# Optimization experiments

Measured on AMD Instinct MI355X. Metric: run time of the kernel, lower is better.

## Reference

```python
import jax, jax.numpy as jnp
import numpy as np

D_MODEL = 1024
N_HEADS = 16
HEAD_DIM = D_MODEL // N_HEADS


def setup_inputs() -> dict:
    key = jax.random.key(0)
    ks = jax.random.split(key, 5)
    scale = 1.0 / np.sqrt(D_MODEL)
    return {
        "x": jax.random.normal(ks[0], (4, 2048, D_MODEL), dtype=jnp.float32),
        "W_q": jax.random.normal(ks[1], (D_MODEL, D_MODEL), dtype=jnp.float32) * scale,
        "W_k": jax.random.normal(ks[2], (D_MODEL, D_MODEL), dtype=jnp.float32) * scale,
        "W_v": jax.random.normal(ks[3], (D_MODEL, D_MODEL), dtype=jnp.float32) * scale,
        "W_o": jax.random.normal(ks[4], (D_MODEL, D_MODEL), dtype=jnp.float32) * scale,
    }


def _split_heads(t):
    # (B, T, d_model) -> (B, H, T, head_dim)
    B, T, _ = t.shape
    return t.reshape(B, T, N_HEADS, HEAD_DIM).transpose(0, 2, 1, 3)


def reference(x, W_q, W_k, W_v, W_o):
    B, T, _ = x.shape
    # torch nn.Linear: y = x @ W.T
    q = _split_heads(x @ W_q.T)
    k = _split_heads(x @ W_k.T)
    v = _split_heads(x @ W_v.T)
    scale = jnp.asarray(np.sqrt(HEAD_DIM), x.dtype)
    # (B, H, T, T) scores, additive causal mask (triu above diagonal = -inf)
    scores = jnp.einsum("bhqd,bhkd->bhqk", q, k) / scale
    causal = jnp.tril(jnp.ones((T, T), dtype=bool))
    scores = jnp.where(causal, scores, jnp.asarray(-jnp.inf, scores.dtype))
    weights = jax.nn.softmax(scores, axis=-1)
    out = jnp.einsum("bhqk,bhkd->bhqd", weights, v)
    out = out.transpose(0, 2, 1, 3).reshape(B, T, D_MODEL)
    out = out @ W_o.T
    return out, k, v
```

## Files before the change

### kernel.cpp

```cpp
#include <hip/hip_runtime.h>
#include <stdint.h>

typedef __bf16 bf16;
typedef __bf16 bf16x8 __attribute__((ext_vector_type(8)));
typedef __bf16 bf16x4 __attribute__((ext_vector_type(4)));
typedef short short4v __attribute__((ext_vector_type(4)));
typedef float f32x4 __attribute__((ext_vector_type(4)));
typedef int v2i __attribute__((ext_vector_type(2)));
typedef uint32_t u32;

#define MFMA_BF16(a, b, c) __builtin_amdgcn_mfma_f32_16x16x32_bf16(a, b, c, 0, 0, 0)
#define MFMA16(a, b, c)                                                   \
  __builtin_amdgcn_mfma_f32_16x16x16bf16_1k(*(const short4v*)&(a),        \
                                            *(const short4v*)&(b), c, 0, 0, 0)

#define TRREAD(dst, va, IMM)                                             \
  asm volatile("ds_read_b64_tr_b16 %0, %1 offset:" #IMM                  \
               : "=v"(dst)                                               \
               : "v"(va))

constexpr int D_MODEL = 1024;
constexpr int T_SEQ = 2048;
constexpr int NH = 16;
constexpr int HD = 64;
constexpr size_t OUT_ELEMS = (size_t)4 * T_SEQ * D_MODEL;
constexpr size_t X_ELEMS = OUT_ELEMS;
constexpr size_t W_ELEMS = (size_t)D_MODEL * D_MODEL;

__device__ __forceinline__ void gload16(const bf16* g, bf16* l) {
  __builtin_amdgcn_global_load_lds(
      (const __attribute__((address_space(1))) unsigned int*)g,
      (__attribute__((address_space(3))) unsigned int*)l, 16, 0, 0);
}

__global__ __launch_bounds__(256) void convert_kernel(
    const float* __restrict__ x, const float* __restrict__ wq,
    const float* __restrict__ wk, const float* __restrict__ wv,
    const float* __restrict__ wo, bf16* __restrict__ dst,
    bf16* __restrict__ wo_b) {
  const size_t nchunk = (X_ELEMS + 4 * W_ELEMS) / 8;
  for (size_t c = (size_t)blockIdx.x * 256 + threadIdx.x; c < nchunk;
       c += (size_t)gridDim.x * 256) {
    const size_t off = c * 8;
    const float* src;
    bf16* d;
    size_t rel;
    if (off < X_ELEMS) {
      src = x;
      rel = off;
      d = dst + off;
    } else {
      const size_t j = off - X_ELEMS;
      const int w = (int)(j >> 20);
      rel = j & (W_ELEMS - 1);
      if (w == 3) {
        if (!wo_b) continue;
        src = wo;
        d = wo_b + rel;
      } else {
        src = (w == 0) ? wq : (w == 1) ? wk : wv;
        d = dst + off;
      }
    }
    const f32x4 a = *(const f32x4*)(src + rel);
    const f32x4 b = *(const f32x4*)(src + rel + 4);
    bf16x8 o;
#pragma unroll
    for (int e = 0; e < 4; ++e) {
      o[e] = (bf16)a[e];
      o[e + 4] = (bf16)b[e];
    }
    *(bf16x8*)d = o;
  }
}

template <bool B_F32>
__global__ __launch_bounds__(256) void gemm2(
    const bf16* __restrict__ A, const bf16* __restrict__ WB,
    const float* __restrict__ WF, int modeBase, bf16* __restrict__ dstB,
    float* __restrict__ dstF1, float* __restrict__ dstF2) {
  const int z = blockIdx.z;
  const int mode = modeBase + z;
  const bf16* Bb = B_F32 ? nullptr : WB + (size_t)z * W_ELEMS;
  const int m0 = blockIdx.y * 128, n0 = blockIdx.x * 128;
  const int tid = threadIdx.x;
  const int wave = tid >> 6, lane = tid & 63;
  const int quad = lane >> 4, c16 = lane & 15;
  const int wr = wave >> 1, wc = wave & 1;

  __shared__ __align__(16) bf16 As[128 * 64];
  __shared__ __align__(16) bf16 Bs[128 * 64];

  f32x4 acc[4][4];
#pragma unroll
  for (int i = 0; i < 4; ++i)
#pragma unroll
    for (int j = 0; j < 4; ++j) acc[i][j] = (f32x4){0.f, 0.f, 0.f, 0.f};

  const int r8 = lane >> 3;
  const int s8 = lane & 7;
  const int ksw = ((s8 ^ r8) * 8);
  const int swA = (c16 & 7);

  for (int k0 = 0; k0 < 1024; k0 += 64) {
    __syncthreads();
#pragma unroll
    for (int c = 0; c < 4; ++c) {
      const int chunk = wave + c * 4;
      const int row = chunk * 8 + r8;
      gload16(A + (size_t)(m0 + row) * 1024 + k0 + ksw, &As[chunk * 512]);
      if (!B_F32)
        gload16(Bb + (size_t)(n0 + row) * 1024 + k0 + ksw, &Bs[chunk * 512]);
    }
    if (B_F32) {
#pragma unroll
      for (int g = 0; g < 4; ++g) {
        const int gi = g * 256 + tid;
        const int row = gi >> 3, s = gi & 7;
        const float* bp = WF + (size_t)(n0 + row) * 1024 + k0 + s * 8;
        const f32x4 b0 = *(const f32x4*)bp;
        const f32x4 b1 = *(const f32x4*)(bp + 4);
        bf16x8 vb;
#pragma unroll
        for (int e = 0; e < 4; ++e) {
          vb[e] = (bf16)b0[e];
          vb[e + 4] = (bf16)b1[e];
        }
        *(bf16x8*)&Bs[row * 64 + ((s ^ (row & 7)) * 8)] = vb;
      }
    }
    asm volatile("s_waitcnt vmcnt(0)" ::: "memory");
    __syncthreads();

#pragma unroll
    for (int kk = 0; kk < 2; ++kk) {
      bf16x8 af[4], bfr[4];
#pragma unroll
      for (int i = 0; i < 4; ++i) {
        const int row = wr * 64 + i * 16 + c16;
        af[i] = *(const bf16x8*)&As[row * 64 + (((quad + kk * 4) ^ swA) * 8)];
      }
#pragma unroll
      for (int j = 0; j < 4; ++j) {
        const int row = wc * 64 + j * 16 + c16;
        bfr[j] = *(const bf16x8*)&Bs[row * 64 + (((quad + kk * 4) ^ swA) * 8)];
      }
#pragma unroll
      for (int i = 0; i < 4; ++i)
#pragma unroll
        for (int j = 0; j < 4; ++j)
          acc[i][j] = MFMA_BF16(af[i], bfr[j], acc[i][j]);
    }
  }

  const int row0 = m0 + wr * 64, col0 = n0 + wc * 64;
#pragma unroll
  for (int i = 0; i < 4; ++i) {
#pragma unroll
    for (int r = 0; r < 4; ++r) {
      const int row = row0 + i * 16 + quad * 4 + r;
      const int b = row >> 11, t = row & 2047;
#pragma unroll
      for (int j = 0; j < 4; ++j) {
        const int cc = col0 + j * 16 + c16;
        const float v = acc[i][j][r];
        if (mode == 0) {
          dstB[(size_t)row * 1024 + cc] = (bf16)v;
        } else if (mode == 3) {
          dstF1[(size_t)row * 1024 + cc] = v;
        } else {
          const int h = cc >> 6, d = cc & 63;
          float* df = (mode == 1) ? dstF1 : dstF2;
          df[((size_t)(b * NH + h) * T_SEQ + t) * HD + d] = v;
        }
      }
    }
  }
}

__device__ __forceinline__ void load_kv(const float* Kg, const float* Vg,
                                        int t0, int st, int sd,
                                        f32x4 pk[2][2], f32x4 pv[2][2]) {
#pragma unroll
  for (int p = 0; p < 2; ++p) {
    const float* kp = Kg + (size_t)(t0 + p * 32 + st) * HD + sd * 8;
    pk[p][0] = *(const f32x4*)kp;
    pk[p][1] = *(const f32x4*)(kp + 4);
    const float* vp = Vg + (size_t)(t0 + p * 32 + st) * HD + sd * 8;
    pv[p][0] = *(const f32x4*)vp;
    pv[p][1] = *(const f32x4*)(vp + 4);
  }
}

__global__ __launch_bounds__(256, 4) void attn_kernel(
    const bf16* __restrict__ Q, const float* __restrict__ K,
    const float* __restrict__ V, bf16* __restrict__ Aout) {
  const int bx = blockIdx.x;
  const int by = blockIdx.y;
  const int r16 = (bx + ((by >> 4) << 2)) & 15;
  const int qt = (r16 < 8) ? r16 : 23 - r16;
  const int b = by >> 4, h = by & 15;
  const int tid = threadIdx.x, wave = tid >> 6, lane = tid & 63;
  const int quad = lane >> 4, c16 = lane & 15;

  __shared__ __align__(16) bf16 Ks[64 * 70];
  __shared__ __align__(16) bf16 Vs[4096];

  const int q0w = qt * 128 + wave * 32;
  const bf16* Qb = Q + ((size_t)b * T_SEQ + q0w) * D_MODEL + h * HD;
  const float* Kg = K + (size_t)by * T_SEQ * HD;
  const float* Vg = V + (size_t)by * T_SEQ * HD;

  bf16x8 aq[2][2];
#pragma unroll
  for (int mt = 0; mt < 2; ++mt) {
    const bf16* qp = Qb + (size_t)(mt * 16 + c16) * D_MODEL + quad * 8;
    aq[mt][0] = *(const bf16x8*)qp;
    aq[mt][1] = *(const bf16x8*)(qp + 32);
  }

  f32x4 O[2][4], racc[2];
#pragma unroll
  for (int mt = 0; mt < 2; ++mt) {
    racc[mt] = (f32x4){0.f, 0.f, 0.f, 0.f};
#pragma unroll
    for (int dj = 0; dj < 4; ++dj) O[mt][dj] = (f32x4){0.f, 0.f, 0.f, 0.f};
  }

  bf16x4 ones4;
#pragma unroll
  for (int e = 0; e < 4; ++e) ones4[e] = (bf16)1.0f;

  const float sc = 0.125f * 1.44269504088896340736f;
  const int nkt = 2 * qt + 2;
  const int st = tid >> 3, sd = tid & 7;
  const u32 vtr =
      (u32)(uintptr_t)(const __attribute__((address_space(3))) bf16*)Vs +
      (u32)lane * 8;

  f32x4 pk[2][2], pv[2][2];
  load_kv(Kg, Vg, 0, st, sd, pk, pv);

  for (int kt = 0; kt < nkt; ++kt) {
    const int t0 = kt * 64;

    __syncthreads();
#pragma unroll
    for (int p = 0; p < 2; ++p) {
      const int t = p * 32 + st;
      bf16x8 kb, vb;
#pragma unroll
      for (int e = 0; e < 4; ++e) {
        kb[e] = (bf16)pk[p][0][e];
        kb[e + 4] = (bf16)pk[p][1][e];
        vb[e] = (bf16)pv[p][0][e];
        vb[e + 4] = (bf16)pv[p][1][e];
      }
      *(bf16x8*)&Ks[t * 70 + sd * 8] = kb;
      *(bf16x8*)&Vs[(((t >> 4) * 4 + (sd >> 1)) * 256) + (t & 15) * 16 +
                    (sd & 1) * 8] = vb;
    }
    if (kt + 1 < nkt) load_kv(Kg, Vg, t0 + 64, st, sd, pk, pv);
    __syncthreads();

    const bool act[2] = {t0 <= q0w + 15, t0 <= q0w + 31};

    bf16x4 ap16[2][4];
#pragma unroll
    for (int j = 0; j < 4; ++j) {
      const bf16* kp = &Ks[(j * 16 + c16) * 70 + quad * 8];
      const bf16x8 ak0 = *(const bf16x8*)kp;
      const bf16x8 ak1 = *(const bf16x8*)(kp + 32);
#pragma unroll
      for (int mt = 0; mt < 2; ++mt) {
        if (!act[mt]) continue;
        f32x4 s = (f32x4){0.f, 0.f, 0.f, 0.f};
        s = MFMA_BF16(ak0, aq[mt][0], s);
        s = MFMA_BF16(ak1, aq[mt][1], s);
        const int trow = t0 + j * 16 + quad * 4;
        const int qcol = q0w + mt * 16 + c16;
        bf16x4 pa;
#pragma unroll
        for (int r = 0; r < 4; ++r)
          pa[r] = (bf16)((trow + r <= qcol) ? exp2f(s[r] * sc) : 0.f);
        ap16[mt][j] = pa;
      }
    }

    if (act[1]) {
#pragma unroll
      for (int mt = 0; mt < 2; ++mt) {
        if (!act[mt]) continue;
#pragma unroll
        for (int j = 0; j < 4; ++j)
          racc[mt] = MFMA16(ap16[mt][j], ones4, racc[mt]);
      }
      v2i bv0, bv1, bv2, bv3;
#define PV_DJ(DJ, O0, O1, O2, O3)                                        \
  {                                                                      \
    TRREAD(bv0, vtr, O0);                                                \
    TRREAD(bv1, vtr, O1);                                                \
    TRREAD(bv2, vtr, O2);                                                \
    TRREAD(bv3, vtr, O3);                                                \
    asm volatile("s_waitcnt lgkmcnt(0)" ::: "memory");                   \
    __builtin_amdgcn_sched_barrier(0);                                   \
    _Pragma("unroll") for (int mt = 0; mt < 2; ++mt) {                   \
      if (act[mt]) {                                                     \
        O[mt][DJ] = MFMA16(ap16[mt][0], bv0, O[mt][DJ]);                 \
        O[mt][DJ] = MFMA16(ap16[mt][1], bv1, O[mt][DJ]);                 \
        O[mt][DJ] = MFMA16(ap16[mt][2], bv2, O[mt][DJ]);                 \
        O[mt][DJ] = MFMA16(ap16[mt][3], bv3, O[mt][DJ]);                 \
      }                                                                  \
    }                                                                    \
  }
      PV_DJ(0, 0, 2048, 4096, 6144)
      PV_DJ(1, 512, 2560, 4608, 6656)
      PV_DJ(2, 1024, 3072, 5120, 7168)
      PV_DJ(3, 1536, 3584, 5632, 7680)
#undef PV_DJ
    }
  }

#pragma unroll
  for (int mt = 0; mt < 2; ++mt) {
    f32x4 inv;
#pragma unroll
    for (int r = 0; r < 4; ++r) inv[r] = 1.f / racc[mt][r];
#pragma unroll
    for (int dj = 0; dj < 4; ++dj)
#pragma unroll
      for (int r = 0; r < 4; ++r) {
        const int q = q0w + mt * 16 + quad * 4 + r;
        Aout[((size_t)b * T_SEQ + q) * D_MODEL + h * HD + dj * 16 + c16] =
            (bf16)(O[mt][dj][r] * inv[r]);
      }
  }
}

extern "C" void kernel_launch(void* const* d_in, const int* in_sizes, int n_in,
                              void* d_out, int out_size, void* d_ws, size_t ws_size,
                              hipStream_t stream) {
  const float* x = (const float*)d_in[0];
  const float* wq = (const float*)d_in[1];
  const float* wk = (const float*)d_in[2];
  const float* wv = (const float*)d_in[3];
  const float* wo = (const float*)d_in[4];

  float* out = (float*)d_out;
  float* kout = out + OUT_ELEMS;
  float* vout = out + 2 * OUT_ELEMS;

  bf16* ws = (bf16*)d_ws;
  bf16* Qbuf = ws;
  bf16* Abuf = ws;

  bf16* cvt = (bf16*)d_out;
  const bf16* xb = cvt;
  const bf16* wb = cvt + X_ELEMS;

  const bool wo_bf = ws_size >= (X_ELEMS + W_ELEMS) * sizeof(bf16);
  bf16* wo_b = wo_bf ? (ws + X_ELEMS) : nullptr;

  convert_kernel<<<dim3(2048), 256, 0, stream>>>(x, wq, wk, wv, wo, cvt, wo_b);
  gemm2<false><<<dim3(8, 64, 3), 256, 0, stream>>>(xb, wb, nullptr, 0, Qbuf,
                                                   kout, vout);
  attn_kernel<<<dim3(16, 64), 256, 0, stream>>>(Qbuf, kout, vout, Abuf);
  if (wo_bf) {
    gemm2<false><<<dim3(8, 64, 1), 256, 0, stream>>>(Abuf, wo_b, nullptr, 3,
                                                     nullptr, out, nullptr);
  } else {
    gemm2<true><<<dim3(8, 64, 1), 256, 0, stream>>>(Abuf, nullptr, wo, 3,
                                                    nullptr, out, nullptr);
  }
}
```

Before: 377.0 us.

## Split attention block into 8 waves of 16 query rows with MFMA priority

Raises the attention block from 256 to 512 threads so each wave owns 16 query rows instead of 32, and each thread stages a single K/V row chunk per tile. This halves per-wave register state (O, ap16, prefetch buffers) and adds more waves to hide latency, including finer-grained causal skipping per 16-row wave. It also raises wave priority around the MFMA section with s_setprio. The cost is that each K/V tile in LDS is reused by fewer rows per wave, more waves wait at each barrier, and the explicit occupancy hint is dropped.

```diff
diff --git a/kernel.cpp b/kernel.cpp
--- a/kernel.cpp
+++ b/kernel.cpp
@@ -178,21 +178,7 @@
   }
 }
 
-__device__ __forceinline__ void load_kv(const float* Kg, const float* Vg,
-                                        int t0, int st, int sd,
-                                        f32x4 pk[2][2], f32x4 pv[2][2]) {
-#pragma unroll
-  for (int p = 0; p < 2; ++p) {
-    const float* kp = Kg + (size_t)(t0 + p * 32 + st) * HD + sd * 8;
-    pk[p][0] = *(const f32x4*)kp;
-    pk[p][1] = *(const f32x4*)(kp + 4);
-    const float* vp = Vg + (size_t)(t0 + p * 32 + st) * HD + sd * 8;
-    pv[p][0] = *(const f32x4*)vp;
-    pv[p][1] = *(const f32x4*)(vp + 4);
-  }
-}
-
-__global__ __launch_bounds__(256, 4) void attn_kernel(
+__global__ __launch_bounds__(512) void attn_kernel(
     const bf16* __restrict__ Q, const float* __restrict__ K,
     const float* __restrict__ V, bf16* __restrict__ Aout) {
   const int bx = blockIdx.x;
@@ -206,26 +192,21 @@
   __shared__ __align__(16) bf16 Ks[64 * 70];
   __shared__ __align__(16) bf16 Vs[4096];
 
-  const int q0w = qt * 128 + wave * 32;
-  const bf16* Qb = Q + ((size_t)b * T_SEQ + q0w) * D_MODEL + h * HD;
+  const int q0w = qt * 128 + wave * 16;
   const float* Kg = K + (size_t)by * T_SEQ * HD;
   const float* Vg = V + (size_t)by * T_SEQ * HD;
 
-  bf16x8 aq[2][2];
-#pragma unroll
-  for (int mt = 0; mt < 2; ++mt) {
-    const bf16* qp = Qb + (size_t)(mt * 16 + c16) * D_MODEL + quad * 8;
-    aq[mt][0] = *(const bf16x8*)qp;
-    aq[mt][1] = *(const bf16x8*)(qp + 32);
-  }
-
-  f32x4 O[2][4], racc[2];
-#pragma unroll
-  for (int mt = 0; mt < 2; ++mt) {
-    racc[mt] = (f32x4){0.f, 0.f, 0.f, 0.f};
-#pragma unroll
-    for (int dj = 0; dj < 4; ++dj) O[mt][dj] = (f32x4){0.f, 0.f, 0.f, 0.f};
-  }
+  bf16x8 aq[2];
+  {
+    const bf16* qp =
+        Q + ((size_t)b * T_SEQ + q0w + c16) * D_MODEL + h * HD + quad * 8;
+    aq[0] = *(const bf16x8*)qp;
+    aq[1] = *(const bf16x8*)(qp + 32);
+  }
+
+  f32x4 O[4], racc = (f32x4){0.f, 0.f, 0.f, 0.f};
+#pragma unroll
+  for (int dj = 0; dj < 4; ++dj) O[dj] = (f32x4){0.f, 0.f, 0.f, 0.f};
 
   bf16x4 ones4;
 #pragma unroll
@@ -238,63 +219,65 @@
       (u32)(uintptr_t)(const __attribute__((address_space(3))) bf16*)Vs +
       (u32)lane * 8;
 
-  f32x4 pk[2][2], pv[2][2];
-  load_kv(Kg, Vg, 0, st, sd, pk, pv);
+  f32x4 pk[2], pv[2];
+  {
+    const float* kp = Kg + (size_t)st * HD + sd * 8;
+    pk[0] = *(const f32x4*)kp;
+    pk[1] = *(const f32x4*)(kp + 4);
+    const float* vp = Vg + (size_t)st * HD + sd * 8;
+    pv[0] = *(const f32x4*)vp;
+    pv[1] = *(const f32x4*)(vp + 4);
+  }
 
   for (int kt = 0; kt < nkt; ++kt) {
     const int t0 = kt * 64;
 
     __syncthreads();
-#pragma unroll
-    for (int p = 0; p < 2; ++p) {
-      const int t = p * 32 + st;
+    {
       bf16x8 kb, vb;
 #pragma unroll
       for (int e = 0; e < 4; ++e) {
-        kb[e] = (bf16)pk[p][0][e];
-        kb[e + 4] = (bf16)pk[p][1][e];
-        vb[e] = (bf16)pv[p][0][e];
-        vb[e + 4] = (bf16)pv[p][1][e];
-      }
-      *(bf16x8*)&Ks[t * 70 + sd * 8] = kb;
-      *(bf16x8*)&Vs[(((t >> 4) * 4 + (sd >> 1)) * 256) + (t & 15) * 16 +
+        kb[e] = (bf16)pk[0][e];
+        kb[e + 4] = (bf16)pk[1][e];
+        vb[e] = (bf16)pv[0][e];
+        vb[e + 4] = (bf16)pv[1][e];
+      }
+      *(bf16x8*)&Ks[st * 70 + sd * 8] = kb;
+      *(bf16x8*)&Vs[(((st >> 4) * 4 + (sd >> 1)) * 256) + (st & 15) * 16 +
                     (sd & 1) * 8] = vb;
     }
-    if (kt + 1 < nkt) load_kv(Kg, Vg, t0 + 64, st, sd, pk, pv);
+    if (kt + 1 < nkt) {
+      const float* kp = Kg + (size_t)(t0 + 64 + st) * HD + sd * 8;
+      pk[0] = *(const f32x4*)kp;
+      pk[1] = *(const f32x4*)(kp + 4);
+      const float* vp = Vg + (size_t)(t0 + 64 + st) * HD + sd * 8;
+      pv[0] = *(const f32x4*)vp;
+      pv[1] = *(const f32x4*)(vp + 4);
+    }
     __syncthreads();
 
-    const bool act[2] = {t0 <= q0w + 15, t0 <= q0w + 31};
-
-    bf16x4 ap16[2][4];
-#pragma unroll
-    for (int j = 0; j < 4; ++j) {
-      const bf16* kp = &Ks[(j * 16 + c16) * 70 + quad * 8];
-      const bf16x8 ak0 = *(const bf16x8*)kp;
-      const bf16x8 ak1 = *(const bf16x8*)(kp + 32);
-#pragma unroll
-      for (int mt = 0; mt < 2; ++mt) {
-        if (!act[mt]) continue;
+    if (t0 <= q0w + 15) {
+      bf16x4 ap16[4];
+#pragma unroll
+      for (int j = 0; j < 4; ++j) {
+        const bf16* kp = &Ks[(j * 16 + c16) * 70 + quad * 8];
+        const bf16x8 ak0 = *(const bf16x8*)kp;
+        const bf16x8 ak1 = *(const bf16x8*)(kp + 32);
         f32x4 s = (f32x4){0.f, 0.f, 0.f, 0.f};
-        s = MFMA_BF16(ak0, aq[mt][0], s);
-        s = MFMA_BF16(ak1, aq[mt][1], s);
+        s = MFMA_BF16(ak0, aq[0], s);
+        s = MFMA_BF16(ak1, aq[1], s);
         const int trow = t0 + j * 16 + quad * 4;
-        const int qcol = q0w + mt * 16 + c16;
+        const int qcol = q0w + c16;
         bf16x4 pa;
 #pragma unroll
         for (int r = 0; r < 4; ++r)
           pa[r] = (bf16)((trow + r <= qcol) ? exp2f(s[r] * sc) : 0.f);
-        ap16[mt][j] = pa;
-      }
-    }
-
-    if (act[1]) {
-#pragma unroll
-      for (int mt = 0; mt < 2; ++mt) {
-        if (!act[mt]) continue;
-#pragma unroll
-        for (int j = 0; j < 4; ++j)
-          racc[mt] = MFMA16(ap16[mt][j], ones4, racc[mt]);
-      }
+        ap16[j] = pa;
+      }
+
+      __builtin_amdgcn_s_setprio(1);
+#pragma unroll
+      for (int j = 0; j < 4; ++j) racc = MFMA16(ap16[j], ones4, racc);
       v2i bv0, bv1, bv2, bv3;
 #define PV_DJ(DJ, O0, O1, O2, O3)                                        \
   {                                                                      \
@@ -304,37 +287,31 @@
     TRREAD(bv3, vtr, O3);                                                \
     asm volatile("s_waitcnt lgkmcnt(0)" ::: "memory");                   \
     __builtin_amdgcn_sched_barrier(0);                                   \
-    _Pragma("unroll") for (int mt = 0; mt < 2; ++mt) {                   \
-      if (act[mt]) {                                                     \
-        O[mt][DJ] = MFMA16(ap16[mt][0], bv0, O[mt][DJ]);                 \
-        O[mt][DJ] = MFMA16(ap16[mt][1], bv1, O[mt][DJ]);                 \
-        O[mt][DJ] = MFMA16(ap16[mt][2], bv2, O[mt][DJ]);                 \
-        O[mt][DJ] = MFMA16(ap16[mt][3], bv3, O[mt][DJ]);                 \
-      }                                                                  \
-    }                                                                    \
+    O[DJ] = MFMA16(ap16[0], bv0, O[DJ]);                                 \
+    O[DJ] = MFMA16(ap16[1], bv1, O[DJ]);                                 \
+    O[DJ] = MFMA16(ap16[2], bv2, O[DJ]);                                 \
+    O[DJ] = MFMA16(ap16[3], bv3, O[DJ]);                                 \
   }
       PV_DJ(0, 0, 2048, 4096, 6144)
       PV_DJ(1, 512, 2560, 4608, 6656)
       PV_DJ(2, 1024, 3072, 5120, 7168)
       PV_DJ(3, 1536, 3584, 5632, 7680)
 #undef PV_DJ
-    }
-  }
-
-#pragma unroll
-  for (int mt = 0; mt < 2; ++mt) {
-    f32x4 inv;
-#pragma unroll
-    for (int r = 0; r < 4; ++r) inv[r] = 1.f / racc[mt][r];
-#pragma unroll
-    for (int dj = 0; dj < 4; ++dj)
-#pragma unroll
-      for (int r = 0; r < 4; ++r) {
-        const int q = q0w + mt * 16 + quad * 4 + r;
-        Aout[((size_t)b * T_SEQ + q) * D_MODEL + h * HD + dj * 16 + c16] =
-            (bf16)(O[mt][dj][r] * inv[r]);
-      }
-  }
+      __builtin_amdgcn_s_setprio(0);
+    }
+  }
+
+  f32x4 inv;
+#pragma unroll
+  for (int r = 0; r < 4; ++r) inv[r] = 1.f / racc[r];
+#pragma unroll
+  for (int dj = 0; dj < 4; ++dj)
+#pragma unroll
+    for (int r = 0; r < 4; ++r) {
+      const int q = q0w + quad * 4 + r;
+      Aout[((size_t)b * T_SEQ + q) * D_MODEL + h * HD + dj * 16 + c16] =
+          (bf16)(O[dj][r] * inv[r]);
+    }
 }
 
 extern "C" void kernel_launch(void* const* d_in, const int* in_sizes, int n_in,
@@ -364,7 +341,7 @@
   convert_kernel<<<dim3(2048), 256, 0, stream>>>(x, wq, wk, wv, wo, cvt, wo_b);
   gemm2<false><<<dim3(8, 64, 3), 256, 0, stream>>>(xb, wb, nullptr, 0, Qbuf,
                                                    kout, vout);
-  attn_kernel<<<dim3(16, 64), 256, 0, stream>>>(Qbuf, kout, vout, Abuf);
+  attn_kernel<<<dim3(16, 64), 512, 0, stream>>>(Qbuf, kout, vout, Abuf);
   if (wo_bf) {
     gemm2<false><<<dim3(8, 64, 1), 256, 0, stream>>>(Abuf, wo_b, nullptr, 3,
                                                      nullptr, out, nullptr);
```

New measurement: 476.4 us. +26.4%, slower.

## Double attention KV tile to 128 and skip fully masked 16-row subtiles

Applied to the files above, without the earlier changes.

The attention kernel now stages 128 K/V rows per iteration instead of 64, which halves the number of block-wide barriers and prefetch rounds. The inner loop is restructured per 16-row key subtile, and subtiles entirely above the causal diagonal for the wave are skipped, along with their QK and PV MFMAs. The tradeoff is doubled LDS use and more prefetch registers, which may lower occupancy. There is also a per-subtile branch, and the PV reads now wait on LDS per subtile rather than per output column group.

```diff
diff --git a/kernel.cpp b/kernel.cpp
--- a/kernel.cpp
+++ b/kernel.cpp
@@ -180,9 +180,9 @@
 
 __device__ __forceinline__ void load_kv(const float* Kg, const float* Vg,
                                         int t0, int st, int sd,
-                                        f32x4 pk[2][2], f32x4 pv[2][2]) {
-#pragma unroll
-  for (int p = 0; p < 2; ++p) {
+                                        f32x4 pk[4][2], f32x4 pv[4][2]) {
+#pragma unroll
+  for (int p = 0; p < 4; ++p) {
     const float* kp = Kg + (size_t)(t0 + p * 32 + st) * HD + sd * 8;
     pk[p][0] = *(const f32x4*)kp;
     pk[p][1] = *(const f32x4*)(kp + 4);
@@ -203,8 +203,8 @@
   const int tid = threadIdx.x, wave = tid >> 6, lane = tid & 63;
   const int quad = lane >> 4, c16 = lane & 15;
 
-  __shared__ __align__(16) bf16 Ks[64 * 70];
-  __shared__ __align__(16) bf16 Vs[4096];
+  __shared__ __align__(16) bf16 Ks[128 * 70];
+  __shared__ __align__(16) bf16 Vs[8192];
 
   const int q0w = qt * 128 + wave * 32;
   const bf16* Qb = Q + ((size_t)b * T_SEQ + q0w) * D_MODEL + h * HD;
@@ -232,21 +232,21 @@
   for (int e = 0; e < 4; ++e) ones4[e] = (bf16)1.0f;
 
   const float sc = 0.125f * 1.44269504088896340736f;
-  const int nkt = 2 * qt + 2;
+  const int nkt = qt + 1;
   const int st = tid >> 3, sd = tid & 7;
   const u32 vtr =
       (u32)(uintptr_t)(const __attribute__((address_space(3))) bf16*)Vs +
       (u32)lane * 8;
 
-  f32x4 pk[2][2], pv[2][2];
+  f32x4 pk[4][2], pv[4][2];
   load_kv(Kg, Vg, 0, st, sd, pk, pv);
 
   for (int kt = 0; kt < nkt; ++kt) {
-    const int t0 = kt * 64;
+    const int t0 = kt * 128;
 
     __syncthreads();
 #pragma unroll
-    for (int p = 0; p < 2; ++p) {
+    for (int p = 0; p < 4; ++p) {
       const int t = p * 32 + st;
       bf16x8 kb, vb;
 #pragma unroll
@@ -260,64 +260,62 @@
       *(bf16x8*)&Vs[(((t >> 4) * 4 + (sd >> 1)) * 256) + (t & 15) * 16 +
                     (sd & 1) * 8] = vb;
     }
-    if (kt + 1 < nkt) load_kv(Kg, Vg, t0 + 64, st, sd, pk, pv);
+    if (kt + 1 < nkt) load_kv(Kg, Vg, t0 + 128, st, sd, pk, pv);
     __syncthreads();
 
-    const bool act[2] = {t0 <= q0w + 15, t0 <= q0w + 31};
-
-    bf16x4 ap16[2][4];
-#pragma unroll
-    for (int j = 0; j < 4; ++j) {
-      const bf16* kp = &Ks[(j * 16 + c16) * 70 + quad * 8];
-      const bf16x8 ak0 = *(const bf16x8*)kp;
-      const bf16x8 ak1 = *(const bf16x8*)(kp + 32);
-#pragma unroll
-      for (int mt = 0; mt < 2; ++mt) {
-        if (!act[mt]) continue;
-        f32x4 s = (f32x4){0.f, 0.f, 0.f, 0.f};
-        s = MFMA_BF16(ak0, aq[mt][0], s);
-        s = MFMA_BF16(ak1, aq[mt][1], s);
-        const int trow = t0 + j * 16 + quad * 4;
-        const int qcol = q0w + mt * 16 + c16;
-        bf16x4 pa;
-#pragma unroll
-        for (int r = 0; r < 4; ++r)
-          pa[r] = (bf16)((trow + r <= qcol) ? exp2f(s[r] * sc) : 0.f);
-        ap16[mt][j] = pa;
-      }
-    }
-
-    if (act[1]) {
-#pragma unroll
-      for (int mt = 0; mt < 2; ++mt) {
-        if (!act[mt]) continue;
-#pragma unroll
-        for (int j = 0; j < 4; ++j)
-          racc[mt] = MFMA16(ap16[mt][j], ones4, racc[mt]);
-      }
-      v2i bv0, bv1, bv2, bv3;
-#define PV_DJ(DJ, O0, O1, O2, O3)                                        \
-  {                                                                      \
-    TRREAD(bv0, vtr, O0);                                                \
-    TRREAD(bv1, vtr, O1);                                                \
-    TRREAD(bv2, vtr, O2);                                                \
-    TRREAD(bv3, vtr, O3);                                                \
-    asm volatile("s_waitcnt lgkmcnt(0)" ::: "memory");                   \
-    __builtin_amdgcn_sched_barrier(0);                                   \
-    _Pragma("unroll") for (int mt = 0; mt < 2; ++mt) {                   \
-      if (act[mt]) {                                                     \
-        O[mt][DJ] = MFMA16(ap16[mt][0], bv0, O[mt][DJ]);                 \
-        O[mt][DJ] = MFMA16(ap16[mt][1], bv1, O[mt][DJ]);                 \
-        O[mt][DJ] = MFMA16(ap16[mt][2], bv2, O[mt][DJ]);                 \
-        O[mt][DJ] = MFMA16(ap16[mt][3], bv3, O[mt][DJ]);                 \
-      }                                                                  \
-    }                                                                    \
-  }
-      PV_DJ(0, 0, 2048, 4096, 6144)
-      PV_DJ(1, 512, 2560, 4608, 6656)
-      PV_DJ(2, 1024, 3072, 5120, 7168)
-      PV_DJ(3, 1536, 3584, 5632, 7680)
-#undef PV_DJ
+#pragma unroll
+    for (int j = 0; j < 8; ++j) {
+      const int trow0 = t0 + j * 16;
+      if (trow0 <= q0w + 31) {
+        const bf16* kp = &Ks[(j * 16 + c16) * 70 + quad * 8];
+        const bf16x8 ak0 = *(const bf16x8*)kp;
+        const bf16x8 ak1 = *(const bf16x8*)(kp + 32);
+        const bool act0 = trow0 <= q0w + 15;
+
+        bf16x4 ap[2];
+        {
+          f32x4 s = (f32x4){0.f, 0.f, 0.f, 0.f};
+          s = MFMA_BF16(ak0, aq[1][0], s);
+          s = MFMA_BF16(ak1, aq[1][1], s);
+          const int qcol = q0w + 16 + c16;
+#pragma unroll
+          for (int r = 0; r < 4; ++r)
+            ap[1][r] =
+                (bf16)((trow0 + quad * 4 + r <= qcol) ? exp2f(s[r] * sc) : 0.f);
+        }
+        if (act0) {
+          f32x4 s = (f32x4){0.f, 0.f, 0.f, 0.f};
+          s = MFMA_BF16(ak0, aq[0][0], s);
+          s = MFMA_BF16(ak1, aq[0][1], s);
+          const int qcol = q0w + c16;
+#pragma unroll
+          for (int r = 0; r < 4; ++r)
+            ap[0][r] =
+                (bf16)((trow0 + quad * 4 + r <= qcol) ? exp2f(s[r] * sc) : 0.f);
+        }
+
+        racc[1] = MFMA16(ap[1], ones4, racc[1]);
+        if (act0) racc[0] = MFMA16(ap[0], ones4, racc[0]);
+
+        const u32 vtrj = vtr + (u32)j * 2048;
+        v2i bv0, bv1, bv2, bv3;
+        TRREAD(bv0, vtrj, 0);
+        TRREAD(bv1, vtrj, 512);
+        TRREAD(bv2, vtrj, 1024);
+        TRREAD(bv3, vtrj, 1536);
+        asm volatile("s_waitcnt lgkmcnt(0)" ::: "memory");
+        __builtin_amdgcn_sched_barrier(0);
+        O[1][0] = MFMA16(ap[1], bv0, O[1][0]);
+        O[1][1] = MFMA16(ap[1], bv1, O[1][1]);
+        O[1][2] = MFMA16(ap[1], bv2, O[1][2]);
+        O[1][3] = MFMA16(ap[1], bv3, O[1][3]);
+        if (act0) {
+          O[0][0] = MFMA16(ap[0], bv0, O[0][0]);
+          O[0][1] = MFMA16(ap[0], bv1, O[0][1]);
+          O[0][2] = MFMA16(ap[0], bv2, O[0][2]);
+          O[0][3] = MFMA16(ap[0], bv3, O[0][3]);
+        }
+      }
     }
   }
 
```

Measured after the change: 510.2 us. 35.3% more time.
